# Kernel optimization log

Measured on AMD Instinct MI355X. Metric: run time of the kernel, lower is better.

The kernel has to match this reference:

```python
import jax, jax.numpy as jnp
import numpy as np

MEL = 80      # mel_dim
RED = 2       # reduction factor
D   = 256     # decoder_dim (== enc_output feature dim for dot attention)
E   = 128     # encoder_dim == prenet output dim
PRE = 256     # prenet hidden
B, T, L = 128, 500, 256


def _gru_cell(x, h, w_ih, w_hh, b_ih, b_hh):
    # PyTorch GRUCell math
    gi = x @ w_ih.T + b_ih
    gh = h @ w_hh.T + b_hh
    i_r, i_z, i_n = jnp.split(gi, 3, axis=-1)
    h_r, h_z, h_n = jnp.split(gh, 3, axis=-1)
    r = jax.nn.sigmoid(i_r + h_r)
    z = jax.nn.sigmoid(i_z + h_z)
    n = jnp.tanh(i_n + r * h_n)
    return (1.0 - z) * n + z * h


def setup_inputs() -> dict:
    key = jax.random.key(0)
    ks = jax.random.split(key, 16)
    def p(k, shape, s=0.05):
        return jax.random.normal(k, shape, dtype=jnp.float32) * s
    z = lambda n: jnp.zeros((n,), jnp.float32)
    return {
        'dec_input':  jax.random.normal(ks[0], (B, T, MEL), jnp.float32),
        'enc_output': jax.random.normal(ks[1], (B, L, D), jnp.float32),
        # prenet: mel -> 256 -> 128 (ReLU; dropout omitted for determinism)
        'pre_w1': p(ks[2], (PRE, MEL)), 'pre_b1': z(PRE),
        'pre_w2': p(ks[3], (E, PRE)),   'pre_b2': z(E),
        # attention GRUCell(encoder_dim -> decoder_dim)
        'attn_wih': p(ks[4], (3 * D, E)), 'attn_whh': p(ks[5], (3 * D, D)),
        'attn_bih': z(3 * D), 'attn_bhh': z(3 * D),
        # proj1: 2*decoder_dim -> decoder_dim
        'proj1_w': p(ks[6], (D, 2 * D)), 'proj1_b': z(D),
        # decoder GRUCells
        'rnn1_wih': p(ks[7], (3 * D, D)), 'rnn1_whh': p(ks[8], (3 * D, D)),
        'rnn1_bih': z(3 * D), 'rnn1_bhh': z(3 * D),
        'rnn2_wih': p(ks[9], (3 * D, D)), 'rnn2_whh': p(ks[10], (3 * D, D)),
        'rnn2_bih': z(3 * D), 'rnn2_bhh': z(3 * D),
        # proj2: decoder_dim -> mel_dim * reduction
        'proj2_w': p(ks[11], (MEL * RED, D)), 'proj2_b': z(MEL * RED),
    }


def reference(dec_input, enc_output,
              pre_w1, pre_b1, pre_w2, pre_b2,
              attn_wih, attn_whh, attn_bih, attn_bhh,
              proj1_w, proj1_b,
              rnn1_wih, rnn1_whh, rnn1_bih, rnn1_bhh,
              rnn2_wih, rnn2_whh, rnn2_bih, rnn2_bhh,
              proj2_w, proj2_b):
    b, t, _ = dec_input.shape

    def step(carry, frame):
        h_attn, h1, h2 = carry
        # prenet
        x = jax.nn.relu(frame @ pre_w1.T + pre_b1)
        x = jax.nn.relu(x @ pre_w2.T + pre_b2)
        # attention RNN
        h_attn = _gru_cell(x, h_attn, attn_wih, attn_whh, attn_bih, attn_bhh)
        # Luong dot attention: query = h_attn [b, D]
        scores = jnp.einsum('bd,bld->bl', h_attn, enc_output)   # [b, L]
        align = jax.nn.softmax(scores, axis=-1)
        ctx = jnp.einsum('bl,bld->bd', align, enc_output)        # [b, D]
        dec_in = jnp.concatenate([ctx, h_attn], axis=-1) @ proj1_w.T + proj1_b
        # residual GRU stack
        h1 = _gru_cell(dec_in, h1, rnn1_wih, rnn1_whh, rnn1_bih, rnn1_bhh)
        y1 = dec_in + h1
        h2 = _gru_cell(y1, h2, rnn2_wih, rnn2_whh, rnn2_bih, rnn2_bhh)
        y2 = y1 + h2
        out = y2 @ proj2_w.T + proj2_b                            # [b, MEL*RED]
        return (h_attn, h1, h2), (out, align)

    init = tuple(jnp.zeros((b, D), dec_input.dtype) for _ in range(3))
    _, (outs, aligns) = jax.lax.scan(step, init, jnp.swapaxes(dec_input, 0, 1))
    mel_out = jnp.swapaxes(outs, 0, 1).reshape(b, t * RED, MEL)  # [b, T*RED, MEL]
    alignment = jnp.transpose(aligns, (1, 2, 0))                 # [b, L, T]
    return mel_out, alignment
```

## Files before the change

kernel.cpp:

```cpp
#include <hip/hip_runtime.h>
#include <cmath>

#define B_   128
#define T_   500
#define MEL_ 80
#define RED_ 2
#define D_   256
#define E_   128
#define PRE_ 256
#define L_   256
#define TPB  1024
#define ENC_C 256
#define PTT  10

__device__ __forceinline__ float sigmoidf_(float x) { return 1.f / (1.f + expf(-x)); }
__device__ __forceinline__ float bflo(unsigned u) { return __uint_as_float(u << 16); }
__device__ __forceinline__ float bfhi(unsigned u) { return __uint_as_float(u & 0xFFFF0000u); }
__device__ __forceinline__ float bfval(ushort v) { return __uint_as_float(((unsigned)v) << 16); }
__device__ __forceinline__ ushort f2bf(float f) {
    unsigned u = __float_as_uint(f);
    return (ushort)((u + 0x7FFFu + ((u >> 16) & 1u)) >> 16);
}

__device__ __forceinline__ float acc8(uint4 u, const float* vv, float s) {
    s = fmaf(bflo(u.x), vv[0], s);
    s = fmaf(bfhi(u.x), vv[1], s);
    s = fmaf(bflo(u.y), vv[2], s);
    s = fmaf(bfhi(u.y), vv[3], s);
    s = fmaf(bflo(u.z), vv[4], s);
    s = fmaf(bfhi(u.z), vv[5], s);
    s = fmaf(bflo(u.w), vv[6], s);
    s = fmaf(bfhi(u.w), vv[7], s);
    return s;
}

template<int CH>
__device__ __forceinline__ float dotpk(const ushort* __restrict__ wp, int t, const float* v) {
    const uint4* w = reinterpret_cast<const uint4*>(wp) + (t >> 6) * (CH * 64) + (t & 63);
    float s0 = 0.f, s1 = 0.f, s2 = 0.f, s3 = 0.f;
#pragma unroll 2
    for (int c = 0; c < (CH & ~3); c += 4) {
        uint4 u0 = w[(c + 0) * 64];
        uint4 u1 = w[(c + 1) * 64];
        uint4 u2 = w[(c + 2) * 64];
        uint4 u3 = w[(c + 3) * 64];
        s0 = acc8(u0, v + (c + 0) * 8, s0);
        s1 = acc8(u1, v + (c + 1) * 8, s1);
        s2 = acc8(u2, v + (c + 2) * 8, s2);
        s3 = acc8(u3, v + (c + 3) * 8, s3);
    }
    if (CH & 2) {
        constexpr int c0 = CH & ~3;
        uint4 u0 = w[(c0 + 0) * 64];
        uint4 u1 = w[(c0 + 1) * 64];
        s0 = acc8(u0, v + (c0 + 0) * 8, s0);
        s1 = acc8(u1, v + (c0 + 1) * 8, s1);
    }
    return (s0 + s1) + (s2 + s3);
}

__global__ void pack_bf16_kernel(const float* __restrict__ src,
                                 ushort* __restrict__ dst,
                                 int NT, int CH, int dA, int mA, int mB) {
    int i = blockIdx.x * blockDim.x + threadIdx.x;
    int n = NT * CH * 8;
    if (i >= n) return;
    int i4 = i >> 3, e = i & 7;
    int lane = i4 & 63;
    int q = i4 >> 6;
    int c = q % CH;
    int g = q / CH;
    int t = g * 64 + lane;
    dst[i] = f2bf(src[(t / dA) * mA + (t % dA) * mB + c * 8 + e]);
}

__global__ __launch_bounds__(256) void prenet_gi_kernel(
    const float* __restrict__ dec_input,
    const float* __restrict__ pre_w1, const float* __restrict__ pre_b1,
    const float* __restrict__ pre_w2, const float* __restrict__ pre_b2,
    const float* __restrict__ attn_wih, const float* __restrict__ attn_bih,
    ushort* __restrict__ gi_out,
    int b0)
{
    const int blk = blockIdx.x;
    const int bl  = blk / (T_ / PTT);
    const int b   = b0 + bl;
    const int t0  = (blk % (T_ / PTT)) * PTT;
    const int tid = threadIdx.x;

    __shared__ float fr[PTT][MEL_];
    __shared__ float x1[PTT][PRE_];
    __shared__ float x2[PTT][E_];

    for (int i = tid; i < PTT * MEL_; i += 256) {
        int f = i / MEL_, m = i - f * MEL_;
        fr[f][m] = dec_input[((size_t)b * T_ + t0 + f) * MEL_ + m];
    }
    __syncthreads();

    {
        float acc[PTT];
#pragma unroll
        for (int f = 0; f < PTT; ++f) acc[f] = pre_b1[tid];
        const float4* wr = reinterpret_cast<const float4*>(pre_w1 + tid * MEL_);
        for (int k4 = 0; k4 < MEL_ / 4; ++k4) {
            float4 w = wr[k4];
#pragma unroll
            for (int f = 0; f < PTT; ++f) {
                const float* fp = &fr[f][k4 * 4];
                acc[f] = fmaf(w.x, fp[0], fmaf(w.y, fp[1], fmaf(w.z, fp[2], fmaf(w.w, fp[3], acc[f]))));
            }
        }
#pragma unroll
        for (int f = 0; f < PTT; ++f) x1[f][tid] = fmaxf(acc[f], 0.f);
    }
    __syncthreads();

    if (tid < E_) {
        float acc[PTT];
#pragma unroll
        for (int f = 0; f < PTT; ++f) acc[f] = pre_b2[tid];
        const float4* wr = reinterpret_cast<const float4*>(pre_w2 + tid * PRE_);
        for (int k4 = 0; k4 < PRE_ / 4; ++k4) {
            float4 w = wr[k4];
#pragma unroll
            for (int f = 0; f < PTT; ++f) {
                const float* fp = &x1[f][k4 * 4];
                acc[f] = fmaf(w.x, fp[0], fmaf(w.y, fp[1], fmaf(w.z, fp[2], fmaf(w.w, fp[3], acc[f]))));
            }
        }
#pragma unroll
        for (int f = 0; f < PTT; ++f) x2[f][tid] = fmaxf(acc[f], 0.f);
    }
    __syncthreads();

    for (int r = tid; r < 3 * D_; r += 256) {
        float acc[PTT];
#pragma unroll
        for (int f = 0; f < PTT; ++f) acc[f] = attn_bih[r];
        const float4* wr = reinterpret_cast<const float4*>(attn_wih + r * E_);
        for (int k4 = 0; k4 < E_ / 4; ++k4) {
            float4 w = wr[k4];
#pragma unroll
            for (int f = 0; f < PTT; ++f) {
                const float* fp = &x2[f][k4 * 4];
                acc[f] = fmaf(w.x, fp[0], fmaf(w.y, fp[1], fmaf(w.z, fp[2], fmaf(w.w, fp[3], acc[f]))));
            }
        }
#pragma unroll
        for (int f = 0; f < PTT; ++f)
            gi_out[((size_t)bl * T_ + t0 + f) * (3 * D_) + r] = f2bf(acc[f]);
    }
}

__global__ __launch_bounds__(TPB, 4) void decoder_persist(
    const float* __restrict__ enc_output,
    const ushort* __restrict__ attn_whh, const float* __restrict__ attn_bhh,
    const ushort* __restrict__ proj1_w, const float* __restrict__ proj1_b,
    const ushort* __restrict__ rnn1_wih, const ushort* __restrict__ rnn1_whh,
    const float* __restrict__ rnn1_bih, const float* __restrict__ rnn1_bhh,
    const ushort* __restrict__ rnn2_wih, const ushort* __restrict__ rnn2_whh,
    const float* __restrict__ rnn2_bih, const float* __restrict__ rnn2_bhh,
    const ushort* __restrict__ proj2_w, const float* __restrict__ proj2_b,
    const ushort* __restrict__ gi_g,
    int b0,
    float* __restrict__ mel_out,
    float* __restrict__ align_out)
{
    const int b    = blockIdx.x + b0;
    const int tid  = threadIdx.x;
    const int lane = tid & 63;
    const int wv   = tid >> 6;

    __shared__ __align__(16) ushort s_enc[L_ * ENC_C];
    __shared__ __align__(16) float P[4608];
    __shared__ __align__(16) float P2b[640];
    __shared__ __align__(16) float s_ha[D_];
    __shared__ __align__(16) float s_h1[D_];
    __shared__ __align__(16) float s_h2[D_];
    __shared__ __align__(16) float s_dec[D_];
    __shared__ __align__(16) float s_y1[D_];
    __shared__ __align__(16) float s_y2[D_];
    __shared__ __align__(16) float s_ctx[D_];
    __shared__ __align__(16) float s_al[L_];
    __shared__ float s_pmax[4];
    __shared__ float s_psum[4];

    {
        const float4* eb = reinterpret_cast<const float4*>(enc_output + (size_t)b * L_ * D_);
        for (int i = tid; i < (L_ * D_) / 4; i += TPB) {
            float4 f = eb[i];
            int row = i >> 6;
            int c4  = i & 63;
            int c    = c4 >> 1;
            int half = c4 & 1;
            int slot = (c & 24) | ((c & 7) ^ (row & 7));
            uint2 pk;
            pk.x = (unsigned)f2bf(f.x) | ((unsigned)f2bf(f.y) << 16);
            pk.y = (unsigned)f2bf(f.z) | ((unsigned)f2bf(f.w) << 16);
            *reinterpret_cast<uint2*>(s_enc + row * ENC_C + slot * 8 + half * 4) = pk;
        }
    }
    if (tid < D_) { s_ha[tid] = 0.f; s_h1[tid] = 0.f; s_h2[tid] = 0.f; }
    __syncthreads();

    auto gru_combine = [&](const float* gip, const float* ghp,
                           const float* bih, const float* bhh,
                           float* h, const float* xin, float* y) {
        if (tid < D_) {
            int t0 = tid;
            float gir = gip[2 * t0] + gip[2 * t0 + 1] + bih[t0];
            float giz = gip[2 * (D_ + t0)] + gip[2 * (D_ + t0) + 1] + bih[D_ + t0];
            float gin = gip[2 * (2 * D_ + t0)] + gip[2 * (2 * D_ + t0) + 1] + bih[2 * D_ + t0];
            float ghr = ghp[2 * t0] + ghp[2 * t0 + 1] + bhh[t0];
            float ghz = ghp[2 * (D_ + t0)] + ghp[2 * (D_ + t0) + 1] + bhh[D_ + t0];
            float ghn = ghp[2 * (2 * D_ + t0)] + ghp[2 * (2 * D_ + t0) + 1] + bhh[2 * D_ + t0];
            float r = sigmoidf_(gir + ghr);
            float z = sigmoidf_(giz + ghz);
            float n = tanhf(gin + r * ghn);
            float hn = (1.f - z) * n + z * h[t0];
            h[t0] = hn;
            y[t0] = xin[t0] + hn;
        }
    };

    for (int t = 0; t < T_; ++t) {
        for (int task = tid; task < 4608; task += TPB) {
            const ushort* wP; const float* hv; int u;
            if (task < 1536)      { wP = attn_whh; hv = s_ha; u = task; }
            else if (task < 3072) { wP = rnn1_whh; hv = s_h1; u = task - 1536; }
            else                  { wP = rnn2_whh; hv = s_h2; u = task - 3072; }
            P[task] = dotpk<16>(wP, u, hv + (u & 1) * 128);
        }
        __syncthreads();

        if (tid < D_) {
            const ushort* gp = gi_g + ((size_t)blockIdx.x * T_ + t) * (3 * D_);
            float gir = bfval(gp[tid]);
            float giz = bfval(gp[D_ + tid]);
            float gin = bfval(gp[2 * D_ + tid]);
            float ghr = P[2 * tid] + P[2 * tid + 1] + attn_bhh[tid];
            float ghz = P[2 * (D_ + tid)] + P[2 * (D_ + tid) + 1] + attn_bhh[D_ + tid];
            float ghn = P[2 * (2 * D_ + tid)] + P[2 * (2 * D_ + tid) + 1] + attn_bhh[2 * D_ + tid];
            float r = sigmoidf_(gir + ghr);
            float z = sigmoidf_(giz + ghz);
            float n = tanhf(gin + r * ghn);
            s_ha[tid] = (1.f - z) * n + z * s_ha[tid];
        }
        __syncthreads();

        {
            int p = tid >> 8, l = tid & 255;
            const uint4* rowp = reinterpret_cast<const uint4*>(s_enc + l * ENC_C) + p * 8;
            const float* v = s_ha + p * 64;
            int rot = l & 7;
            float a0 = 0.f, a1 = 0.f, a2 = 0.f, a3 = 0.f;
#pragma unroll
            for (int k = 0; k < 8; k += 4) {
                uint4 u0 = rowp[(k + 0) ^ rot];
                uint4 u1 = rowp[(k + 1) ^ rot];
                uint4 u2 = rowp[(k + 2) ^ rot];
                uint4 u3 = rowp[(k + 3) ^ rot];
                a0 = acc8(u0, v + (k + 0) * 8, a0);
                a1 = acc8(u1, v + (k + 1) * 8, a1);
                a2 = acc8(u2, v + (k + 2) * 8, a2);
                a3 = acc8(u3, v + (k + 3) * 8, a3);
            }
            P[p * 256 + l] = (a0 + a1) + (a2 + a3);
        }
        __syncthreads();
        float sc = 0.f, e = 0.f;
        if (tid < L_) {
            sc = P[tid] + P[256 + tid] + P[512 + tid] + P[768 + tid];
            float m = sc;
            for (int o = 32; o > 0; o >>= 1) m = fmaxf(m, __shfl_xor(m, o, 64));
            if (lane == 0) s_pmax[wv] = m;
        }
        __syncthreads();
        if (tid < L_) {
            float mm = fmaxf(fmaxf(s_pmax[0], s_pmax[1]), fmaxf(s_pmax[2], s_pmax[3]));
            e = expf(sc - mm);
            float sm = e;
            for (int o = 32; o > 0; o >>= 1) sm += __shfl_xor(sm, o, 64);
            if (lane == 0) s_psum[wv] = sm;
        }
        __syncthreads();
        if (tid < L_) {
            float denom = s_psum[0] + s_psum[1] + s_psum[2] + s_psum[3];
            float al = e / denom;
            s_al[tid] = al;
            align_out[((size_t)b * L_ + tid) * T_ + t] = al;
        }
        __syncthreads();

        {
            int p = tid >> 8, d = tid & 255;
            int chigh = (d >> 3) & 24, clow = (d >> 3) & 7, el = d & 7;
            const float* alp = s_al + p * 64;
            float a0 = 0.f, a1 = 0.f;
            for (int l8 = 0; l8 < 8; ++l8) {
                const ushort* rb = s_enc + (p * 64 + l8 * 8) * ENC_C;
                const float* al8 = alp + l8 * 8;
#pragma unroll
                for (int dr = 0; dr < 8; ++dr) {
                    int slot = chigh | (clow ^ dr);
                    float vv = bfval(rb[dr * ENC_C + slot * 8 + el]);
                    if (dr & 1) a1 = fmaf(al8[dr], vv, a1);
                    else        a0 = fmaf(al8[dr], vv, a0);
                }
            }
            P[p * 256 + d] = a0 + a1;
        }
        __syncthreads();
        if (tid < D_)
            s_ctx[tid] = P[tid] + P[256 + tid] + P[512 + tid] + P[768 + tid];
        __syncthreads();

        {
            int p = tid >> 8;
            const float* v = (p < 2) ? (s_ctx + p * 128) : (s_ha + (p - 2) * 128);
            P[tid] = dotpk<16>(proj1_w, tid, v);
        }
        __syncthreads();
        if (tid < D_)
            s_dec[tid] = P[tid] + P[256 + tid] + P[512 + tid] + P[768 + tid] + proj1_b[tid];
        __syncthreads();

        for (int task = tid; task < 1536; task += TPB)
            P[task] = dotpk<16>(rnn1_wih, task, s_dec + (task & 1) * 128);
        __syncthreads();
        gru_combine(P, P + 1536, rnn1_bih, rnn1_bhh, s_h1, s_dec, s_y1);
        __syncthreads();

        for (int task = tid; task < 1536; task += TPB)
            P[task] = dotpk<16>(rnn2_wih, task, s_y1 + (task & 1) * 128);
        __syncthreads();
        gru_combine(P, P + 3072, rnn2_bih, rnn2_bhh, s_h2, s_y1, s_y2);
        __syncthreads();

        if (tid < 640)
            P2b[tid] = dotpk<8>(proj2_w, tid, s_y2 + (tid & 3) * 64);
        __syncthreads();
        if (tid < MEL_ * RED_) {
            float s = P2b[4 * tid] + P2b[4 * tid + 1] + P2b[4 * tid + 2] + P2b[4 * tid + 3] + proj2_b[tid];
            mel_out[(size_t)b * (T_ * RED_ * MEL_) + (size_t)t * (MEL_ * RED_) + tid] = s;
        }
    }
}

extern "C" void kernel_launch(void* const* d_in, const int* in_sizes, int n_in,
                              void* d_out, int out_size, void* d_ws, size_t ws_size,
                              hipStream_t stream) {
    const float* dec_input = (const float*)d_in[0];
    const float* enc_output= (const float*)d_in[1];
    const float* pre_w1    = (const float*)d_in[2];
    const float* pre_b1    = (const float*)d_in[3];
    const float* pre_w2    = (const float*)d_in[4];
    const float* pre_b2    = (const float*)d_in[5];
    const float* attn_wih  = (const float*)d_in[6];
    const float* attn_whh  = (const float*)d_in[7];
    const float* attn_bih  = (const float*)d_in[8];
    const float* attn_bhh  = (const float*)d_in[9];
    const float* proj1_w   = (const float*)d_in[10];
    const float* proj1_b   = (const float*)d_in[11];
    const float* rnn1_wih  = (const float*)d_in[12];
    const float* rnn1_whh  = (const float*)d_in[13];
    const float* rnn1_bih  = (const float*)d_in[14];
    const float* rnn1_bhh  = (const float*)d_in[15];
    const float* rnn2_wih  = (const float*)d_in[16];
    const float* rnn2_whh  = (const float*)d_in[17];
    const float* rnn2_bih  = (const float*)d_in[18];
    const float* rnn2_bhh  = (const float*)d_in[19];
    const float* proj2_w   = (const float*)d_in[20];
    const float* proj2_b   = (const float*)d_in[21];

    float* mel   = (float*)d_out;
    float* align = (float*)d_out + (size_t)B_ * T_ * RED_ * MEL_;

    const int n_whh   = 3 * D_ * D_;
    const int n_proj1 = D_ * 2 * D_;
    const int n_proj2 = MEL_ * RED_ * D_;

    ushort* w = (ushort*)d_ws;
    ushort* c_attn_whh = w; w += n_whh;
    ushort* c_proj1    = w; w += n_proj1;
    ushort* c_rnn1_wih = w; w += n_whh;
    ushort* c_rnn1_whh = w; w += n_whh;
    ushort* c_rnn2_wih = w; w += n_whh;
    ushort* c_rnn2_whh = w; w += n_whh;
    ushort* c_proj2    = w; w += n_proj2;
    ushort* c_gi       = w;

    auto pack = [&](const float* src, ushort* dst, int NT, int CH, int dA, int mA, int mB) {
        int n = NT * CH * 8;
        pack_bf16_kernel<<<dim3((n + 255) / 256), dim3(256), 0, stream>>>(
            src, dst, NT, CH, dA, mA, mB);
    };
    pack(attn_whh, c_attn_whh, 1536, 16, 2,   256, 128);
    pack(proj1_w,  c_proj1,    1024, 16, 256, 128, 512);
    pack(rnn1_wih, c_rnn1_wih, 1536, 16, 2,   256, 128);
    pack(rnn1_whh, c_rnn1_whh, 1536, 16, 2,   256, 128);
    pack(rnn2_wih, c_rnn2_wih, 1536, 16, 2,   256, 128);
    pack(rnn2_whh, c_rnn2_whh, 1536, 16, 2,   256, 128);
    pack(proj2_w,  c_proj2,    640,  8,  4,   256, 64);

    const size_t packed_elems = (size_t)(w - (ushort*)d_ws);
    const size_t gi_per_b = (size_t)T_ * 3 * D_;
    size_t avail = (ws_size / 2 > packed_elems) ? (ws_size / 2 - packed_elems) : 0;
    int bchunk = (int)(avail / gi_per_b);
    if (bchunk > B_) bchunk = B_;
    if (bchunk < 1)  bchunk = 1;

    for (int b0 = 0; b0 < B_; b0 += bchunk) {
        int nb = (b0 + bchunk <= B_) ? bchunk : (B_ - b0);
        prenet_gi_kernel<<<dim3(nb * (T_ / PTT)), dim3(256), 0, stream>>>(
            dec_input, pre_w1, pre_b1, pre_w2, pre_b2, attn_wih, attn_bih,
            c_gi, b0);
        decoder_persist<<<dim3(nb), dim3(TPB), 0, stream>>>(
            enc_output,
            c_attn_whh, attn_bhh,
            c_proj1, proj1_b,
            c_rnn1_wih, c_rnn1_whh, rnn1_bih, rnn1_bhh,
            c_rnn2_wih, c_rnn2_whh, rnn2_bih, rnn2_bhh,
            c_proj2, proj2_b,
            c_gi, b0,
            mel, align);
    }
}
```

Measured before the change: 15.53 ms.

## Repack GRU weights so each thread computes two output rows per dot product

Adds a paired-row weight packing (pack_pq_kernel) and a dotpq routine in which each thread produces two output rows, reusing each loaded input-vector chunk for both. The recurrent and input GRU matvecs and proj1 move to this scheme with different K-split factors, and the partial sums are reduced across 2, 4 or 8 parts. The shared partial buffers are reorganised into A/G arrays, and the GRU combines are inlined with ctx stored directly in s_y1. This is meant to cut shared-memory vector reads and task count per step, at the cost of fewer parallel tasks for some matvecs, longer serial dot products per thread, and an extra barrier at the end of each step.

```diff
diff --git a/kernel.cpp b/kernel.cpp
--- a/kernel.cpp
+++ b/kernel.cpp
@@ -32,6 +32,21 @@
     s = fmaf(bflo(u.w), vv[6], s);
     s = fmaf(bfhi(u.w), vv[7], s);
     return s;
+}
+
+template<int PS>
+__device__ __forceinline__ float2 dotpq(const ushort* __restrict__ wp, int t, const float* v) {
+    const uint4* w = reinterpret_cast<const uint4*>(wp) + (t >> 6) * (2 * PS * 64) + (t & 63);
+    float e0 = 0.f, e1 = 0.f, o0 = 0.f, o1 = 0.f;
+#pragma unroll 4
+    for (int k = 0; k < PS; ++k) {
+        uint4 we = w[(2 * k) * 64];
+        uint4 wo = w[(2 * k + 1) * 64];
+        const float* vv = v + k * 8;
+        if (k & 1) { e1 = acc8(we, vv, e1); o1 = acc8(wo, vv, o1); }
+        else       { e0 = acc8(we, vv, e0); o0 = acc8(wo, vv, o0); }
+    }
+    return make_float2(e0 + e1, o0 + o1);
 }
 
 template<int CH>
@@ -49,14 +64,29 @@
         s2 = acc8(u2, v + (c + 2) * 8, s2);
         s3 = acc8(u3, v + (c + 3) * 8, s3);
     }
-    if (CH & 2) {
-        constexpr int c0 = CH & ~3;
-        uint4 u0 = w[(c0 + 0) * 64];
-        uint4 u1 = w[(c0 + 1) * 64];
-        s0 = acc8(u0, v + (c0 + 0) * 8, s0);
-        s1 = acc8(u1, v + (c0 + 1) * 8, s1);
-    }
     return (s0 + s1) + (s2 + s3);
+}
+
+__global__ void pack_pq_kernel(const float* __restrict__ src,
+                               ushort* __restrict__ dst,
+                               int R, int K, int PS) {
+    int i = blockIdx.x * blockDim.x + threadIdx.x;
+    int n = R * K;
+    if (i >= n) return;
+    int e = i & 7;
+    int j = i >> 3;
+    int CH = 2 * PS;
+    int g = j / (CH * 64);
+    int rem = j - g * (CH * 64);
+    int c = rem >> 6;
+    int lane = rem & 63;
+    int t = g * 64 + lane;
+    int nparts = K / (8 * PS);
+    int rp = t / nparts;
+    int part = t - rp * nparts;
+    int row = 2 * rp + (c & 1);
+    int colc = part * PS + (c >> 1);
+    dst[i] = f2bf(src[row * K + colc * 8 + e]);
 }
 
 __global__ void pack_bf16_kernel(const float* __restrict__ src,
@@ -167,21 +197,21 @@
     float* __restrict__ mel_out,
     float* __restrict__ align_out)
 {
-    const int b    = blockIdx.x + b0;
     const int tid  = threadIdx.x;
     const int lane = tid & 63;
     const int wv   = tid >> 6;
+    const int bl   = blockIdx.x;
+    const int b    = b0 + bl;
 
     __shared__ __align__(16) ushort s_enc[L_ * ENC_C];
-    __shared__ __align__(16) float P[4608];
-    __shared__ __align__(16) float P2b[640];
+    __shared__ __align__(16) float A[3072];
+    __shared__ __align__(16) float G[3072];
     __shared__ __align__(16) float s_ha[D_];
     __shared__ __align__(16) float s_h1[D_];
     __shared__ __align__(16) float s_h2[D_];
     __shared__ __align__(16) float s_dec[D_];
     __shared__ __align__(16) float s_y1[D_];
     __shared__ __align__(16) float s_y2[D_];
-    __shared__ __align__(16) float s_ctx[D_];
     __shared__ __align__(16) float s_al[L_];
     __shared__ float s_pmax[4];
     __shared__ float s_psum[4];
@@ -204,44 +234,35 @@
     if (tid < D_) { s_ha[tid] = 0.f; s_h1[tid] = 0.f; s_h2[tid] = 0.f; }
     __syncthreads();
 
-    auto gru_combine = [&](const float* gip, const float* ghp,
-                           const float* bih, const float* bhh,
-                           float* h, const float* xin, float* y) {
+    for (int t = 0; t < T_; ++t) {
+        for (int task = tid; task < 3072; task += TPB) {
+            if (task < 1536) {
+                int q = task & 3, rp = task >> 2;
+                float2 r = dotpq<8>(attn_whh, task, s_ha + q * 64);
+                A[(2 * rp) * 4 + q]     = r.x;
+                A[(2 * rp + 1) * 4 + q] = r.y;
+            } else {
+                int u = task - 1536;
+                const ushort* wm; const float* h; float* Gb;
+                if (u < 768) { wm = rnn1_whh; h = s_h1; Gb = G; }
+                else         { u -= 768; wm = rnn2_whh; h = s_h2; Gb = G + 1536; }
+                int half = u & 1, rp = u >> 1;
+                float2 r = dotpq<16>(wm, u, h + half * 128);
+                Gb[(2 * rp) * 2 + half]     = r.x;
+                Gb[(2 * rp + 1) * 2 + half] = r.y;
+            }
+        }
+        __syncthreads();
+
         if (tid < D_) {
-            int t0 = tid;
-            float gir = gip[2 * t0] + gip[2 * t0 + 1] + bih[t0];
-            float giz = gip[2 * (D_ + t0)] + gip[2 * (D_ + t0) + 1] + bih[D_ + t0];
-            float gin = gip[2 * (2 * D_ + t0)] + gip[2 * (2 * D_ + t0) + 1] + bih[2 * D_ + t0];
-            float ghr = ghp[2 * t0] + ghp[2 * t0 + 1] + bhh[t0];
-            float ghz = ghp[2 * (D_ + t0)] + ghp[2 * (D_ + t0) + 1] + bhh[D_ + t0];
-            float ghn = ghp[2 * (2 * D_ + t0)] + ghp[2 * (2 * D_ + t0) + 1] + bhh[2 * D_ + t0];
-            float r = sigmoidf_(gir + ghr);
-            float z = sigmoidf_(giz + ghz);
-            float n = tanhf(gin + r * ghn);
-            float hn = (1.f - z) * n + z * h[t0];
-            h[t0] = hn;
-            y[t0] = xin[t0] + hn;
-        }
-    };
-
-    for (int t = 0; t < T_; ++t) {
-        for (int task = tid; task < 4608; task += TPB) {
-            const ushort* wP; const float* hv; int u;
-            if (task < 1536)      { wP = attn_whh; hv = s_ha; u = task; }
-            else if (task < 3072) { wP = rnn1_whh; hv = s_h1; u = task - 1536; }
-            else                  { wP = rnn2_whh; hv = s_h2; u = task - 3072; }
-            P[task] = dotpk<16>(wP, u, hv + (u & 1) * 128);
-        }
-        __syncthreads();
-
-        if (tid < D_) {
-            const ushort* gp = gi_g + ((size_t)blockIdx.x * T_ + t) * (3 * D_);
+            const ushort* gp = gi_g + ((size_t)bl * T_ + t) * (3 * D_);
             float gir = bfval(gp[tid]);
             float giz = bfval(gp[D_ + tid]);
             float gin = bfval(gp[2 * D_ + tid]);
-            float ghr = P[2 * tid] + P[2 * tid + 1] + attn_bhh[tid];
-            float ghz = P[2 * (D_ + tid)] + P[2 * (D_ + tid) + 1] + attn_bhh[D_ + tid];
-            float ghn = P[2 * (2 * D_ + tid)] + P[2 * (2 * D_ + tid) + 1] + attn_bhh[2 * D_ + tid];
+            int r0 = tid * 4, r1 = (D_ + tid) * 4, r2 = (2 * D_ + tid) * 4;
+            float ghr = ((A[r0] + A[r0 + 1]) + (A[r0 + 2] + A[r0 + 3])) + attn_bhh[tid];
+            float ghz = ((A[r1] + A[r1 + 1]) + (A[r1 + 2] + A[r1 + 3])) + attn_bhh[D_ + tid];
+            float ghn = ((A[r2] + A[r2 + 1]) + (A[r2 + 2] + A[r2 + 3])) + attn_bhh[2 * D_ + tid];
             float r = sigmoidf_(gir + ghr);
             float z = sigmoidf_(giz + ghz);
             float n = tanhf(gin + r * ghn);
@@ -266,12 +287,12 @@
                 a2 = acc8(u2, v + (k + 2) * 8, a2);
                 a3 = acc8(u3, v + (k + 3) * 8, a3);
             }
-            P[p * 256 + l] = (a0 + a1) + (a2 + a3);
+            A[p * 256 + l] = (a0 + a1) + (a2 + a3);
         }
         __syncthreads();
         float sc = 0.f, e = 0.f;
         if (tid < L_) {
-            sc = P[tid] + P[256 + tid] + P[512 + tid] + P[768 + tid];
+            sc = A[tid] + A[256 + tid] + A[512 + tid] + A[768 + tid];
             float m = sc;
             for (int o = 32; o > 0; o >>= 1) m = fmaxf(m, __shfl_xor(m, o, 64));
             if (lane == 0) s_pmax[wv] = m;
@@ -309,42 +330,86 @@
                     else        a0 = fmaf(al8[dr], vv, a0);
                 }
             }
-            P[p * 256 + d] = a0 + a1;
+            A[p * 256 + d] = a0 + a1;
         }
         __syncthreads();
         if (tid < D_)
-            s_ctx[tid] = P[tid] + P[256 + tid] + P[512 + tid] + P[768 + tid];
+            s_y1[tid] = A[tid] + A[256 + tid] + A[512 + tid] + A[768 + tid];
         __syncthreads();
 
         {
-            int p = tid >> 8;
-            const float* v = (p < 2) ? (s_ctx + p * 128) : (s_ha + (p - 2) * 128);
-            P[tid] = dotpk<16>(proj1_w, tid, v);
-        }
-        __syncthreads();
-        if (tid < D_)
-            s_dec[tid] = P[tid] + P[256 + tid] + P[512 + tid] + P[768 + tid] + proj1_b[tid];
-        __syncthreads();
-
-        for (int task = tid; task < 1536; task += TPB)
-            P[task] = dotpk<16>(rnn1_wih, task, s_dec + (task & 1) * 128);
-        __syncthreads();
-        gru_combine(P, P + 1536, rnn1_bih, rnn1_bhh, s_h1, s_dec, s_y1);
-        __syncthreads();
-
-        for (int task = tid; task < 1536; task += TPB)
-            P[task] = dotpk<16>(rnn2_wih, task, s_y1 + (task & 1) * 128);
-        __syncthreads();
-        gru_combine(P, P + 3072, rnn2_bih, rnn2_bhh, s_h2, s_y1, s_y2);
+            int part = tid & 7, rp = tid >> 3;
+            const float* v = (part < 4) ? (s_y1 + part * 64) : (s_ha + (part - 4) * 64);
+            float2 r = dotpq<8>(proj1_w, tid, v);
+            A[(2 * rp) * 8 + part]     = r.x;
+            A[(2 * rp + 1) * 8 + part] = r.y;
+        }
+        __syncthreads();
+        if (tid < D_) {
+            float s = proj1_b[tid];
+#pragma unroll
+            for (int p = 0; p < 8; ++p) s += A[tid * 8 + p];
+            s_dec[tid] = s;
+        }
+        __syncthreads();
+
+        for (int task = tid; task < 1536; task += TPB) {
+            int q = task & 3, rp = task >> 2;
+            float2 r = dotpq<8>(rnn1_wih, task, s_dec + q * 64);
+            A[(2 * rp) * 4 + q]     = r.x;
+            A[(2 * rp + 1) * 4 + q] = r.y;
+        }
+        __syncthreads();
+        if (tid < D_) {
+            int r0 = tid * 4, r1 = (D_ + tid) * 4, r2 = (2 * D_ + tid) * 4;
+            float gir = ((A[r0] + A[r0 + 1]) + (A[r0 + 2] + A[r0 + 3])) + rnn1_bih[tid];
+            float giz = ((A[r1] + A[r1 + 1]) + (A[r1 + 2] + A[r1 + 3])) + rnn1_bih[D_ + tid];
+            float gin = ((A[r2] + A[r2 + 1]) + (A[r2 + 2] + A[r2 + 3])) + rnn1_bih[2 * D_ + tid];
+            float ghr = G[2 * tid] + G[2 * tid + 1] + rnn1_bhh[tid];
+            float ghz = G[2 * (D_ + tid)] + G[2 * (D_ + tid) + 1] + rnn1_bhh[D_ + tid];
+            float ghn = G[2 * (2 * D_ + tid)] + G[2 * (2 * D_ + tid) + 1] + rnn1_bhh[2 * D_ + tid];
+            float r = sigmoidf_(gir + ghr);
+            float z = sigmoidf_(giz + ghz);
+            float n = tanhf(gin + r * ghn);
+            float hn = (1.f - z) * n + z * s_h1[tid];
+            s_h1[tid] = hn;
+            s_y1[tid] = s_dec[tid] + hn;
+        }
+        __syncthreads();
+
+        for (int task = tid; task < 1536; task += TPB) {
+            int q = task & 3, rp = task >> 2;
+            float2 r = dotpq<8>(rnn2_wih, task, s_y1 + q * 64);
+            A[(2 * rp) * 4 + q]     = r.x;
+            A[(2 * rp + 1) * 4 + q] = r.y;
+        }
+        __syncthreads();
+        if (tid < D_) {
+            const float* Gb = G + 1536;
+            int r0 = tid * 4, r1 = (D_ + tid) * 4, r2 = (2 * D_ + tid) * 4;
+            float gir = ((A[r0] + A[r0 + 1]) + (A[r0 + 2] + A[r0 + 3])) + rnn2_bih[tid];
+            float giz = ((A[r1] + A[r1 + 1]) + (A[r1 + 2] + A[r1 + 3])) + rnn2_bih[D_ + tid];
+            float gin = ((A[r2] + A[r2 + 1]) + (A[r2 + 2] + A[r2 + 3])) + rnn2_bih[2 * D_ + tid];
+            float ghr = Gb[2 * tid] + Gb[2 * tid + 1] + rnn2_bhh[tid];
+            float ghz = Gb[2 * (D_ + tid)] + Gb[2 * (D_ + tid) + 1] + rnn2_bhh[D_ + tid];
+            float ghn = Gb[2 * (2 * D_ + tid)] + Gb[2 * (2 * D_ + tid) + 1] + rnn2_bhh[2 * D_ + tid];
+            float r = sigmoidf_(gir + ghr);
+            float z = sigmoidf_(giz + ghz);
+            float n = tanhf(gin + r * ghn);
+            float hn = (1.f - z) * n + z * s_h2[tid];
+            s_h2[tid] = hn;
+            s_y2[tid] = s_y1[tid] + hn;
+        }
         __syncthreads();
 
         if (tid < 640)
-            P2b[tid] = dotpk<8>(proj2_w, tid, s_y2 + (tid & 3) * 64);
+            A[tid] = dotpk<8>(proj2_w, tid, s_y2 + (tid & 3) * 64);
         __syncthreads();
         if (tid < MEL_ * RED_) {
-            float s = P2b[4 * tid] + P2b[4 * tid + 1] + P2b[4 * tid + 2] + P2b[4 * tid + 3] + proj2_b[tid];
+            float s = A[4 * tid] + A[4 * tid + 1] + A[4 * tid + 2] + A[4 * tid + 3] + proj2_b[tid];
             mel_out[(size_t)b * (T_ * RED_ * MEL_) + (size_t)t * (MEL_ * RED_) + tid] = s;
         }
+        __syncthreads();
     }
 }
 
@@ -391,23 +456,26 @@
     ushort* c_proj2    = w; w += n_proj2;
     ushort* c_gi       = w;
 
-    auto pack = [&](const float* src, ushort* dst, int NT, int CH, int dA, int mA, int mB) {
-        int n = NT * CH * 8;
+    auto packpq = [&](const float* src, ushort* dst, int R, int K, int PS) {
+        int n = R * K;
+        pack_pq_kernel<<<dim3((n + 255) / 256), dim3(256), 0, stream>>>(src, dst, R, K, PS);
+    };
+    packpq(attn_whh, c_attn_whh, 768, 256, 8);
+    packpq(rnn1_whh, c_rnn1_whh, 768, 256, 16);
+    packpq(rnn2_whh, c_rnn2_whh, 768, 256, 16);
+    packpq(rnn1_wih, c_rnn1_wih, 768, 256, 8);
+    packpq(rnn2_wih, c_rnn2_wih, 768, 256, 8);
+    packpq(proj1_w,  c_proj1,    256, 512, 8);
+    {
+        int n = 640 * 8 * 8;
         pack_bf16_kernel<<<dim3((n + 255) / 256), dim3(256), 0, stream>>>(
-            src, dst, NT, CH, dA, mA, mB);
-    };
-    pack(attn_whh, c_attn_whh, 1536, 16, 2,   256, 128);
-    pack(proj1_w,  c_proj1,    1024, 16, 256, 128, 512);
-    pack(rnn1_wih, c_rnn1_wih, 1536, 16, 2,   256, 128);
-    pack(rnn1_whh, c_rnn1_whh, 1536, 16, 2,   256, 128);
-    pack(rnn2_wih, c_rnn2_wih, 1536, 16, 2,   256, 128);
-    pack(rnn2_whh, c_rnn2_whh, 1536, 16, 2,   256, 128);
-    pack(proj2_w,  c_proj2,    640,  8,  4,   256, 64);
-
-    const size_t packed_elems = (size_t)(w - (ushort*)d_ws);
+            proj2_w, c_proj2, 640, 8, 4, 256, 64);
+    }
+
     const size_t gi_per_b = (size_t)T_ * 3 * D_;
-    size_t avail = (ws_size / 2 > packed_elems) ? (ws_size / 2 - packed_elems) : 0;
-    int bchunk = (int)(avail / gi_per_b);
+    size_t used = (size_t)((char*)c_gi - (char*)d_ws);
+    size_t avail = (ws_size > used) ? (ws_size - used) : 0;
+    int bchunk = (int)(avail / (gi_per_b * sizeof(ushort)));
     if (bchunk > B_) bchunk = B_;
     if (bchunk < 1)  bchunk = 1;
 
```

New measurement: 18.40 ms. +18.5%, slower.
